# Kernel tuning notes

Measured on AMD Instinct MI355X. Metric: run time of the kernel, lower is better.

## Reference

```python
import jax, jax.numpy as jnp
import numpy as np

EPS = 1e-8
INV_SQRT = 1.0 / np.sqrt(1.0 + EPS)  # 1/sqrt(|k|+eps), |k|=1 for both hyp and sph


def layernorm(x, w, b, eps=1e-5):
    m = jnp.mean(x, axis=-1, keepdims=True)
    v = jnp.mean((x - m) ** 2, axis=-1, keepdims=True)
    return (x - m) * jax.lax.rsqrt(v + eps) * w + b


def setup_inputs() -> dict:
    key = jax.random.key(0)
    B, S, D, H = 4, 1024, 512, 8
    d = D // H
    FF = 2048
    ks = jax.random.split(key, 12)
    s_attn = 1.0 / np.sqrt(d)
    s_d = 1.0 / np.sqrt(D)
    s_ff = 1.0 / np.sqrt(FF)
    return {
        "x": jax.random.normal(ks[0], (B, S, D), jnp.float32),
        "Wq": jax.random.normal(ks[1], (H, d, d), jnp.float32) * s_attn,
        "Wk": jax.random.normal(ks[2], (H, d, d), jnp.float32) * s_attn,
        "Wv": jax.random.normal(ks[3], (H, d, d), jnp.float32) * s_attn,
        "gw": jnp.ones((H, 3), jnp.float32) / 3.0,
        "temp": jnp.ones((H,), jnp.float32),
        "Wo": jax.random.normal(ks[4], (D, D), jnp.float32) * s_d,
        "bo": jnp.zeros((D,), jnp.float32),
        "ln1_w": jnp.ones((D,), jnp.float32),
        "ln1_b": jnp.zeros((D,), jnp.float32),
        "ln2_w": jnp.ones((D,), jnp.float32),
        "ln2_b": jnp.zeros((D,), jnp.float32),
        "W1": jax.random.normal(ks[5], (FF, D), jnp.float32) * s_d,
        "b1": jnp.zeros((FF,), jnp.float32),
        "W2": jax.random.normal(ks[6], (D, FF), jnp.float32) * s_ff,
        "b2": jnp.zeros((D,), jnp.float32),
    }


def reference(x, Wq, Wk, Wv, gw, temp, Wo, bo, ln1_w, ln1_b, ln2_w, ln2_b, W1, b1, W2, b2):
    B, S, D = x.shape
    H = Wq.shape[0]
    d = D // H

    h = layernorm(x, ln1_w, ln1_b)
    xh = h.reshape(B, S, H, d).transpose(0, 2, 1, 3)  # [B,H,S,d]
    # nn.Linear: y = x @ W^T
    q = jnp.einsum("bhsd,hed->bhse", xh, Wq)
    k = jnp.einsum("bhsd,hed->bhse", xh, Wk)
    v = jnp.einsum("bhsd,hed->bhse", xh, Wv)

    qsq = jnp.sum(q * q, axis=-1)  # [B,H,S] == ||q||^2
    ksq = jnp.sum(k * k, axis=-1)
    qk = jnp.einsum("bhsd,bhtd->bhst", q, k)
    # ||q-k||^2 via expansion (same math as sum(diff^2), avoids [B,H,S,S,d])
    dsq = jnp.maximum(qsq[..., :, None] + ksq[..., None, :] - 2.0 * qk, 0.0)
    euc = jnp.sqrt(dsq + EPS)

    denom = (1.0 - qsq)[..., :, None] * (1.0 - ksq)[..., None, :] + EPS
    cosh_arg = jnp.clip(1.0 + 2.0 * dsq / denom, 1.0, 1e6)
    hyp = jnp.arccosh(cosh_arg) * INV_SQRT

    qn = jnp.sqrt(qsq)
    kn = jnp.sqrt(ksq)
    cos_angle = qk / ((qn + EPS)[..., :, None] * (kn + EPS)[..., None, :])
    cos_angle = jnp.clip(cos_angle, -1.0 + EPS, 1.0 - EPS)
    sph = jnp.arccos(cos_angle) * INV_SQRT

    w = jax.nn.softmax(gw, axis=-1)  # [H,3] per-head geometry mixing
    comb = (
        w[:, 0, None, None] * hyp
        + w[:, 1, None, None] * euc
        + w[:, 2, None, None] * sph
    )
    sim = -comb * temp[None, :, None, None]
    attn = jax.nn.softmax(sim, axis=-1)
    out = jnp.einsum("bhst,bhtd->bhsd", attn, v)
    out = out.transpose(0, 2, 1, 3).reshape(B, S, D)
    attn_out = out @ Wo.T + bo

    x = x + attn_out  # dropout=0 (eval)
    h2 = layernorm(x, ln2_w, ln2_b)
    ff = jax.nn.gelu(h2 @ W1.T + b1, approximate=False) @ W2.T + b2
    return x + ff, w
```

## Files before the change

kernel.cpp:

```cpp
#include <hip/hip_runtime.h>
#include <hip/hip_bf16.h>
#include <math.h>

typedef __attribute__((ext_vector_type(4))) float f32x4;
typedef __attribute__((ext_vector_type(8))) short bf16x8;
typedef unsigned short u16;
typedef unsigned int u32;

typedef f32x4  __attribute__((may_alias)) f32x4a;
typedef bf16x8 __attribute__((may_alias)) bf16x8a;
typedef uint2  __attribute__((may_alias)) uint2a;

__device__ __forceinline__ u16 bfbits(float f) {
  union { __hip_bfloat16 h; u16 u; } cv;
  cv.h = __float2bfloat16(f);
  return cv.u;
}
__device__ __forceinline__ float rcp_r(float x)  { return __builtin_amdgcn_rcpf(x); }
__device__ __forceinline__ float sqrt_r(float x) { return __builtin_amdgcn_sqrtf(x); }
__device__ __forceinline__ float log2_r(float x) { return __builtin_amdgcn_logf(x); }
__device__ __forceinline__ float exp2_r(float x) { return __builtin_amdgcn_exp2f(x); }
__device__ __forceinline__ float rsq_r(float x)  { return __builtin_amdgcn_rsqf(x); }
__device__ __forceinline__ u32 cvt_pk_bf16(float lo, float hi) {
  u32 r;
  asm("v_cvt_pk_bf16_f32 %0, %1, %2" : "=v"(r) : "v"(lo), "v"(hi));
  return r;
}
typedef const __attribute__((address_space(1))) unsigned int* gas_t;
typedef __attribute__((address_space(3))) unsigned int* las_t;
__device__ __forceinline__ void gload_lds16(const u16* g, u16* l) {
  __builtin_amdgcn_global_load_lds((gas_t)g, (las_t)l, 16, 0, 0);
}

__global__ __launch_bounds__(256) void convert_weights(
    const float* __restrict__ wq, const float* __restrict__ wk, const float* __restrict__ wv,
    const float* __restrict__ wo, const float* __restrict__ w1, const float* __restrict__ w2,
    u16* __restrict__ owq, u16* __restrict__ owk, u16* __restrict__ owv,
    u16* __restrict__ owo, u16* __restrict__ ow1, u16* __restrict__ ow2) {
  int i = blockIdx.x * 256 + threadIdx.x;
  const float* src; u16* dst; int base;
  if (i < 8192)        { src = wq; dst = owq; base = 0; }
  else if (i < 16384)  { src = wk; dst = owk; base = 8192; }
  else if (i < 24576)  { src = wv; dst = owv; base = 16384; }
  else if (i < 90112)  { src = wo; dst = owo; base = 24576; }
  else if (i < 352256) { src = w1; dst = ow1; base = 90112; }
  else                 { src = w2; dst = ow2; base = 352256; }
  int li = i - base;
  float4 v = reinterpret_cast<const float4*>(src)[li];
  ushort4 o;
  o.x = bfbits(v.x); o.y = bfbits(v.y); o.z = bfbits(v.z); o.w = bfbits(v.w);
  reinterpret_cast<ushort4*>(dst)[li] = o;
}

__global__ __launch_bounds__(128) void ln_kernel(const float* __restrict__ x,
    const float* __restrict__ w, const float* __restrict__ b, u16* __restrict__ out) {
  int row = blockIdx.x, tid = threadIdx.x;
  float4 v = reinterpret_cast<const float4*>(x + row * 512)[tid];
  float s  = v.x + v.y + v.z + v.w;
  float s2 = v.x*v.x + v.y*v.y + v.z*v.z + v.w*v.w;
  #pragma unroll
  for (int o = 32; o > 0; o >>= 1) { s += __shfl_down(s, o); s2 += __shfl_down(s2, o); }
  __shared__ float sm[4];
  if ((tid & 63) == 0) { sm[(tid >> 6)*2] = s; sm[(tid >> 6)*2 + 1] = s2; }
  __syncthreads();
  float ts = sm[0] + sm[2], ts2 = sm[1] + sm[3];
  float mean = ts * (1.f/512.f);
  float var  = ts2 * (1.f/512.f) - mean*mean;
  float rstd = rsq_r(var + 1e-5f);
  float4 wv = reinterpret_cast<const float4*>(w)[tid];
  float4 bv = reinterpret_cast<const float4*>(b)[tid];
  ushort4 o;
  o.x = bfbits((v.x-mean)*rstd*wv.x + bv.x);
  o.y = bfbits((v.y-mean)*rstd*wv.y + bv.y);
  o.z = bfbits((v.z-mean)*rstd*wv.z + bv.z);
  o.w = bfbits((v.w-mean)*rstd*wv.w + bv.w);
  reinterpret_cast<ushort4*>(out + row * 512)[tid] = o;
}

__global__ __launch_bounds__(256) void qkv_kernel(const u16* __restrict__ h1,
    const u16* __restrict__ wqb, const u16* __restrict__ wkb, const u16* __restrict__ wvb,
    u16* __restrict__ q, u16* __restrict__ k, u16* __restrict__ vt,
    float* __restrict__ qsq, float* __restrict__ qom, float* __restrict__ qrs,
    float* __restrict__ ksq, float* __restrict__ kom, float* __restrict__ krs) {
  int mt = blockIdx.x, head = blockIdx.y;
  int wave = threadIdx.x >> 6, lane = threadIdx.x & 63;
  int lr = lane & 15, lg = lane >> 4;
  int m0 = mt * 64 + wave * 16;
  __shared__ u16 qlds[4][16*72];
  const u16* xr = h1 + (m0 + lr) * 512 + head * 64 + lg * 8;
  bf16x8 a0 = *reinterpret_cast<const bf16x8a*>(xr);
  bf16x8 a1 = *reinterpret_cast<const bf16x8a*>(xr + 32);
  int bq = m0 >> 10;
  int s0 = m0 & 1023;
  int bh = (bq << 3) + head;
  #pragma unroll 1
  for (int mat = 0; mat < 3; ++mat) {
    const u16* W = (mat == 0 ? wqb : mat == 1 ? wkb : wvb) + head * 4096;
    f32x4 acc[4];
    #pragma unroll
    for (int c = 0; c < 4; c++)
      #pragma unroll
      for (int j = 0; j < 4; j++) acc[c][j] = 0.f;
    #pragma unroll
    for (int c = 0; c < 4; c++) {
      const u16* wr = W + (c*16 + lr) * 64 + lg * 8;
      bf16x8 b0 = *reinterpret_cast<const bf16x8a*>(wr);
      bf16x8 b1 = *reinterpret_cast<const bf16x8a*>(wr + 32);
      acc[c] = __builtin_amdgcn_mfma_f32_16x16x32_bf16(a0, b0, acc[c], 0, 0, 0);
      acc[c] = __builtin_amdgcn_mfma_f32_16x16x32_bf16(a1, b1, acc[c], 0, 0, 0);
    }
    if (mat == 2) {
      #pragma unroll
      for (int c = 0; c < 4; c++) {
        ushort4 st;
        st.x = bfbits(acc[c][0]); st.y = bfbits(acc[c][1]);
        st.z = bfbits(acc[c][2]); st.w = bfbits(acc[c][3]);
        *reinterpret_cast<ushort4*>(&vt[(bh*64 + c*16 + lr) * 1024 + s0 + 4*lg]) = st;
      }
    } else {
      u16* dst = (mat == 0 ? q : k);
      float* sq = (mat == 0 ? qsq : ksq);
      float* om = (mat == 0 ? qom : kom);
      float* rs = (mat == 0 ? qrs : krs);
      float ss[4] = {0.f, 0.f, 0.f, 0.f};
      u16* tile = &qlds[wave][0];
      #pragma unroll
      for (int c = 0; c < 4; c++)
        #pragma unroll
        for (int j = 0; j < 4; j++) {
          float vv = acc[c][j];
          tile[(4*lg + j)*72 + c*16 + lr] = bfbits(vv);
          ss[j] += vv * vv;
        }
      #pragma unroll
      for (int j = 0; j < 4; j++) {
        #pragma unroll
        for (int o = 1; o < 16; o <<= 1) ss[j] += __shfl_xor(ss[j], o);
      }
      if (lr == 0) {
        #pragma unroll
        for (int j = 0; j < 4; j++) {
          float v = ss[j];
          int idx = bh*1024 + s0 + 4*lg + j;
          sq[idx] = v;
          om[idx] = rcp_r(1.f - v);
          rs[idx] = rsq_r(v);
        }
      }
      int row = lane >> 2, ch = lane & 3;
      bf16x8 r0 = *reinterpret_cast<const bf16x8a*>(&tile[row*72 + ch*16]);
      bf16x8 r1 = *reinterpret_cast<const bf16x8a*>(&tile[row*72 + ch*16 + 8]);
      u16* dp = dst + (size_t)(bh*1024 + s0 + row)*64 + ch*16;
      *reinterpret_cast<bf16x8a*>(dp) = r0;
      *reinterpret_cast<bf16x8a*>(dp + 8) = r1;
    }
  }
}

__global__ __launch_bounds__(512, 4) void attn_kernel(
    const u16* __restrict__ q, const u16* __restrict__ k, const u16* __restrict__ vt,
    const float* __restrict__ qsqA, const float* __restrict__ qomA, const float* __restrict__ qrsA,
    const float* __restrict__ ksqA, const float* __restrict__ komA, const float* __restrict__ krsA,
    const float* __restrict__ gw, const float* __restrict__ temp,
    u16* __restrict__ attnb) {
  int bh = blockIdx.y;
  int b = bh >> 3, head = bh & 7;
  int tid = threadIdx.x;
  int wave = tid >> 6;
  int wq = wave & 1;
  int split = wave >> 1;
  int lane = tid & 63;
  int lr = lane & 15, lg = lane >> 4;
  int q0 = blockIdx.x * 32 + wq * 16;

  const u16* qp = q  + bh * 65536;
  const u16* kp = k  + bh * 65536;
  const u16* vp = vt + bh * 65536;

  __shared__ float ks_s[1024], kom_s[1024], rkn_s[1024];
  __shared__ __align__(16) u16 umem[5120];
  u16* pw = umem + wave * 640;

  for (int i = tid; i < 1024; i += 512) {
    ks_s[i]  = ksqA[(bh << 10) + i];
    kom_s[i] = komA[(bh << 10) + i];
    rkn_s[i] = krsA[(bh << 10) + i];
  }
  __syncthreads();

  float g0 = gw[head*3], g1 = gw[head*3+1], g2 = gw[head*3+2];
  float gm = fmaxf(g0, fmaxf(g1, g2));
  float e0 = __expf(g0-gm), e1 = __expf(g1-gm), e2 = __expf(g2-gm);
  float gi = rcp_r(e0 + e1 + e2);
  float tp = temp[head];
  const float LOG2E = 1.4426950408889634f;
  float chn = -e0*gi*tp;
  float cen = -e1*gi*tp*LOG2E;
  float csn = -e2*gi*tp*LOG2E;

  const u16* qr = qp + (q0 + lr) * 64 + lg * 8;
  bf16x8 aq0 = *reinterpret_cast<const bf16x8a*>(qr);
  bf16x8 aq1 = *reinterpret_cast<const bf16x8a*>(qr + 32);
  float qs   = qsqA[(bh << 10) + q0 + lr];
  float qom2 = 2.f * qomA[(bh << 10) + q0 + lr];
  float rqn  = qrsA[(bh << 10) + q0 + lr];

  f32x4 acc[4];
  #pragma unroll
  for (int c = 0; c < 4; c++)
    #pragma unroll
    for (int j = 0; j < 4; j++) acc[c][j] = 0.f;
  float psum0 = 0.f, psum1 = 0.f;

  for (int it = 0; it < 8; ++it) {
    int t0 = split * 256 + it * 32;
    const u16* kr = kp + (t0 + lr) * 64 + lg * 8;
    bf16x8 k00 = *reinterpret_cast<const bf16x8a*>(kr);
    bf16x8 k01 = *reinterpret_cast<const bf16x8a*>(kr + 32);
    bf16x8 k10 = *reinterpret_cast<const bf16x8a*>(kr + 1024);
    bf16x8 k11 = *reinterpret_cast<const bf16x8a*>(kr + 1024 + 32);
    f32x4 s0, s1;
    #pragma unroll
    for (int j = 0; j < 4; j++) { s0[j] = 0.f; s1[j] = 0.f; }
    s0 = __builtin_amdgcn_mfma_f32_16x16x32_bf16(k00, aq0, s0, 0, 0, 0);
    s0 = __builtin_amdgcn_mfma_f32_16x16x32_bf16(k01, aq1, s0, 0, 0, 0);
    s1 = __builtin_amdgcn_mfma_f32_16x16x32_bf16(k10, aq0, s1, 0, 0, 0);
    s1 = __builtin_amdgcn_mfma_f32_16x16x32_bf16(k11, aq1, s1, 0, 0, 0);

    f32x4 kq0 = *reinterpret_cast<const f32x4a*>(&ks_s[t0 + 4*lg]);
    f32x4 kq1 = *reinterpret_cast<const f32x4a*>(&ks_s[t0 + 16 + 4*lg]);
    f32x4 ko0 = *reinterpret_cast<const f32x4a*>(&kom_s[t0 + 4*lg]);
    f32x4 ko1 = *reinterpret_cast<const f32x4a*>(&kom_s[t0 + 16 + 4*lg]);
    f32x4 rk0 = *reinterpret_cast<const f32x4a*>(&rkn_s[t0 + 4*lg]);
    f32x4 rk1 = *reinterpret_cast<const f32x4a*>(&rkn_s[t0 + 16 + 4*lg]);

    float pv0[4], pv1[4];
    #pragma unroll
    for (int tc = 0; tc < 2; tc++) {
      f32x4 sv = tc ? s1 : s0;
      f32x4 kq = tc ? kq1 : kq0;
      f32x4 ko = tc ? ko1 : ko0;
      f32x4 rk = tc ? rk1 : rk0;
      float* pv = tc ? pv1 : pv0;
      #pragma unroll
      for (int j = 0; j < 4; j++) {
        float qk  = sv[j];
        float dsq = fmaxf(fmaf(qk, -2.f, qs + kq[j]), 0.f);
        float euc = sqrt_r(dsq);
        float u   = dsq * qom2 * ko[j];
        u = fminf(fmaxf(u, 0.f), 999999.f);
        float u2 = u + u;
        float sr = sqrt_r(fmaf(u, u, u2));
        float hyp2 = log2_r((u + 1.f) + sr);
        float ca = qk * rqn * rk[j];
        ca = fminf(fmaxf(ca, -1.f), 1.f);
        float aa = fabsf(ca);
        float pp = fmaf(aa, -0.0187293f, 0.0742610f);
        pp = fmaf(aa, pp, -0.2121144f);
        pp = fmaf(aa, pp, 1.5707288f);
        float rr = sqrt_r(1.f - aa) * pp;
        float sph = ca < 0.f ? 3.14159265358979f - rr : rr;
        float sim2 = fmaf(chn, hyp2, fmaf(cen, euc, csn * sph));
        float p = exp2_r(sim2);
        if (tc) psum1 += p; else psum0 += p;
        pv[j] = p;
      }
    }
    u32 w0 = cvt_pk_bf16(pv0[0], pv0[1]);
    u32 w1 = cvt_pk_bf16(pv0[2], pv0[3]);
    u32 w2 = cvt_pk_bf16(pv1[0], pv1[1]);
    u32 w3 = cvt_pk_bf16(pv1[2], pv1[3]);
    *reinterpret_cast<uint2a*>(pw + lr*40 + 4*lg)      = make_uint2(w0, w1);
    *reinterpret_cast<uint2a*>(pw + lr*40 + 16 + 4*lg) = make_uint2(w2, w3);
    bf16x8 pa = *reinterpret_cast<const bf16x8a*>(pw + lr*40 + lg*8);
    #pragma unroll
    for (int c = 0; c < 4; c++) {
      bf16x8 av = *reinterpret_cast<const bf16x8a*>(vp + (c*16 + lr)*1024 + t0 + lg*8);
      acc[c] = __builtin_amdgcn_mfma_f32_16x16x32_bf16(av, pa, acc[c], 0, 0, 0);
    }
  }

  float lt = psum0 + psum1;
  lt += __shfl_xor(lt, 16);
  lt += __shfl_xor(lt, 32);

  float* fa = (float*)umem;
  __syncthreads();
  #pragma unroll 1
  for (int s = 1; s <= 3; ++s) {
    int base = (wq*64 + lane)*20;
    if (split == s) {
      #pragma unroll
      for (int c = 0; c < 4; c++)
        *reinterpret_cast<f32x4a*>(fa + base + c*4) = acc[c];
      fa[base + 16] = lt;
    }
    __syncthreads();
    if (split == 0) {
      #pragma unroll
      for (int c = 0; c < 4; c++)
        acc[c] += *reinterpret_cast<const f32x4a*>(fa + base + c*4);
      lt += fa[base + 16];
    }
    __syncthreads();
  }
  if (split == 0) {
    float rl = rcp_r(lt);
    #pragma unroll
    for (int c = 0; c < 4; c++) {
      ushort4 st;
      st.x = bfbits(acc[c][0]*rl); st.y = bfbits(acc[c][1]*rl);
      st.z = bfbits(acc[c][2]*rl); st.w = bfbits(acc[c][3]*rl);
      *reinterpret_cast<ushort4*>(
          &attnb[(size_t)((b << 10) + q0 + lr) * 512 + head*64 + c*16 + 4*lg]) = st;
    }
  }
}

template<int K, int KS, int BM, int BN, int MODE>
__global__ __launch_bounds__(256, 2) void gemm_kernel(
    const u16* __restrict__ X, const u16* __restrict__ W,
    const float* __restrict__ bias, const float* __restrict__ res,
    float* __restrict__ outf, float* __restrict__ outf2, u16* __restrict__ outb) {
  constexpr int NS  = (MODE == 1) ? 2048 : 512;
  constexpr int WM  = (BM == 128 && BN == 128) ? 64 : 32;
  constexpr int WN  = (BN == 128 || BM == 128) ? 64 : 32;
  constexpr int NFR = WM / 16;
  constexpr int NFC = WN / 16;
  constexpr int NWC = BN / WN;
  constexpr int ACH = (BM * 4) / 256;
  constexpr int BCH = (BN * 4) / 256;
  __shared__ u16 As[BM * 32];
  __shared__ u16 Bs[BN * 32];
  int tid = threadIdx.x;
  int wave = tid >> 6, lane = tid & 63;
  int lr = lane & 15, lg = lane >> 4;
  int wr = (NWC == 2) ? (wave >> 1) : wave;
  int wc = (NWC == 2) ? (wave & 1) : 0;
  int m0 = blockIdx.x * BM, n0 = blockIdx.y * BN;
  const u16* Xp = X;
  const u16* Wp = W;
  if constexpr (MODE == 3) { Xp += blockIdx.z * K; Wp += blockIdx.z * K; }
  f32x4 acc[NFR][NFC];
  #pragma unroll
  for (int fr = 0; fr < NFR; fr++)
    #pragma unroll
    for (int fc = 0; fc < NFC; fc++)
      #pragma unroll
      for (int j = 0; j < 4; j++) acc[fr][fc][j] = 0.f;
  const u16* Ag[ACH]; u16* Al[ACH];
  const u16* Bg[BCH]; u16* Bl[BCH];
  #pragma unroll
  for (int i = 0; i < ACH; i++) {
    int cb = i * 256 + wave * 64;
    int c  = cb + lane;
    int row = c >> 2;
    int col = ((c & 3) ^ (row & 3)) << 3;
    Ag[i] = Xp + (size_t)(m0 + row) * KS + col;
    Al[i] = As + cb * 8;
  }
  #pragma unroll
  for (int i = 0; i < BCH; i++) {
    int cb = i * 256 + wave * 64;
    int c  = cb + lane;
    int row = c >> 2;
    int col = ((c & 3) ^ (row & 3)) << 3;
    Bg[i] = Wp + (size_t)(n0 + row) * KS + col;
    Bl[i] = Bs + cb * 8;
  }
  int rdcol = ((lg ^ (lr & 3)) << 3);
  for (int k0 = 0; k0 < K; k0 += 32) {
    __syncthreads();
    #pragma unroll
    for (int i = 0; i < ACH; i++) gload_lds16(Ag[i] + k0, Al[i]);
    #pragma unroll
    for (int i = 0; i < BCH; i++) gload_lds16(Bg[i] + k0, Bl[i]);
    __syncthreads();
    bf16x8 af[NFR], bf_[NFC];
    #pragma unroll
    for (int fr = 0; fr < NFR; fr++)
      af[fr] = *reinterpret_cast<const bf16x8a*>(As + (wr*WM + fr*16 + lr)*32 + rdcol);
    #pragma unroll
    for (int fc = 0; fc < NFC; fc++)
      bf_[fc] = *reinterpret_cast<const bf16x8a*>(Bs + (wc*WN + fc*16 + lr)*32 + rdcol);
    #pragma unroll
    for (int fr = 0; fr < NFR; fr++)
      #pragma unroll
      for (int fc = 0; fc < NFC; fc++)
        acc[fr][fc] = __builtin_amdgcn_mfma_f32_16x16x32_bf16(af[fr], bf_[fc], acc[fr][fc], 0, 0, 0);
  }
  float* po = nullptr;
  bool z0 = true;
  if constexpr (MODE == 3) { z0 = (blockIdx.z == 0); po = z0 ? outf : outf2; }
  #pragma unroll
  for (int fr = 0; fr < NFR; fr++)
    #pragma unroll
    for (int fc = 0; fc < NFC; fc++) {
      int col = n0 + wc*WN + fc*16 + lr;
      float bb = (MODE == 3) ? 0.f : bias[col];
      #pragma unroll
      for (int j = 0; j < 4; j++) {
        int row = m0 + wr*WM + fr*16 + 4*lg + j;
        float v = acc[fr][fc][j] + bb;
        if constexpr (MODE == 0) {
          outf[(size_t)row*NS + col] = v + res[(size_t)row*NS + col];
        } else if constexpr (MODE == 1) {
          float t = v * fmaf(v*v, 0.035677408137f, 0.7978845608f);
          float g = v * rcp_r(1.f + exp2_r(-2.8853900817779268f * t));
          outb[(size_t)row*NS + col] = bfbits(g);
        } else {
          if (z0) v += bias[col] + res[(size_t)row*512 + col];
          po[(size_t)row*512 + col] = v;
        }
      }
    }
}

__global__ __launch_bounds__(256) void ff2_combine(
    const float* __restrict__ p0, const float* __restrict__ p1,
    float* __restrict__ out, const float* __restrict__ gw, float* __restrict__ wout) {
  int i = blockIdx.x * 256 + threadIdx.x;
  float4 a = reinterpret_cast<const float4*>(p0)[i];
  float4 b = reinterpret_cast<const float4*>(p1)[i];
  float4 o;
  o.x = a.x + b.x;
  o.y = a.y + b.y;
  o.z = a.z + b.z;
  o.w = a.w + b.w;
  reinterpret_cast<float4*>(out)[i] = o;
  if (blockIdx.x == 0 && threadIdx.x < 8) {
    int h = threadIdx.x;
    float a0 = gw[h*3], a1 = gw[h*3+1], a2 = gw[h*3+2];
    float m = fmaxf(a0, fmaxf(a1, a2));
    float x0 = __expf(a0-m), x1 = __expf(a1-m), x2 = __expf(a2-m);
    float inv = rcp_r(x0 + x1 + x2);
    wout[h*3+0] = x0*inv; wout[h*3+1] = x1*inv; wout[h*3+2] = x2*inv;
  }
}

extern "C" void kernel_launch(void* const* d_in, const int* in_sizes, int n_in,
                              void* d_out, int out_size, void* d_ws, size_t ws_size,
                              hipStream_t stream) {
  const float* x    = (const float*)d_in[0];
  const float* Wq   = (const float*)d_in[1];
  const float* Wk   = (const float*)d_in[2];
  const float* Wv   = (const float*)d_in[3];
  const float* gw   = (const float*)d_in[4];
  const float* temp = (const float*)d_in[5];
  const float* Wo   = (const float*)d_in[6];
  const float* bo   = (const float*)d_in[7];
  const float* ln1w = (const float*)d_in[8];
  const float* ln1b = (const float*)d_in[9];
  const float* ln2w = (const float*)d_in[10];
  const float* ln2b = (const float*)d_in[11];
  const float* W1   = (const float*)d_in[12];
  const float* b1   = (const float*)d_in[13];
  const float* W2   = (const float*)d_in[14];
  const float* b2   = (const float*)d_in[15];

  char* ws = (char*)d_ws;
  u16*  wqb  = (u16*)(ws + 0);
  u16*  wkb  = (u16*)(ws + 65536);
  u16*  wvb  = (u16*)(ws + 131072);
  u16*  wob  = (u16*)(ws + 196608);
  u16*  w1b  = (u16*)(ws + 720896);
  u16*  w2b  = (u16*)(ws + 2818048);
  u16*  h1b  = (u16*)(ws + 4915200);
  u16*  qb   = (u16*)(ws + 9109504);
  u16*  kb   = (u16*)(ws + 13303808);
  u16*  vtb  = (u16*)(ws + 17498112);
  float* qsq = (float*)(ws + 21692416);
  float* ksq = (float*)(ws + 21823488);
  float* qom = (float*)(ws + 21954560);
  float* qrs = (float*)(ws + 22085632);
  float* kom = (float*)(ws + 22216704);
  float* krs = (float*)(ws + 22347776);
  u16*  attnb= (u16*)(ws + 22478848);
  float* x1  = (float*)(ws + 26673152);
  u16*  h2b  = (u16*)(ws + 35061760);
  float* p1f = (float*)(ws + 35061760);
  u16*  gb   = (u16*)(ws + 4915200);

  float* outf = (float*)d_out;
  float* wout = outf + 4096*512;

  convert_weights<<<2400, 256, 0, stream>>>(Wq, Wk, Wv, Wo, W1, W2,
                                            wqb, wkb, wvb, wob, w1b, w2b);
  ln_kernel<<<4096, 128, 0, stream>>>(x, ln1w, ln1b, h1b);
  qkv_kernel<<<dim3(64, 8), 256, 0, stream>>>(h1b, wqb, wkb, wvb, qb, kb, vtb,
                                              qsq, qom, qrs, ksq, kom, krs);
  attn_kernel<<<dim3(32, 32), 512, 0, stream>>>(qb, kb, vtb, qsq, qom, qrs,
                                                ksq, kom, krs, gw, temp, attnb);
  gemm_kernel<512, 512, 64, 64, 0><<<dim3(64, 8), 256, 0, stream>>>(
      attnb, wob, bo, x, x1, nullptr, nullptr);
  ln_kernel<<<4096, 128, 0, stream>>>(x1, ln2w, ln2b, h2b);
  gemm_kernel<512, 512, 128, 128, 1><<<dim3(32, 16), 256, 0, stream>>>(
      h2b, w1b, b1, nullptr, nullptr, nullptr, gb);
  gemm_kernel<1024, 2048, 128, 64, 3><<<dim3(32, 8, 2), 256, 0, stream>>>(
      gb, w2b, b2, x1, outf, p1f, nullptr);
  ff2_combine<<<2048, 256, 0, stream>>>(outf, p1f, outf, gw, wout);
}
```

Before: 229.8 us.

## Fuse Wo projection with LayerNorm2, merge prep kernels, drop FF2 split-K

Merges weight conversion, LayerNorm1 and the gate-weight softmax into one prep launch. Fuses the Wo GEMM with residual add and LayerNorm2 in a new kernel where each block computes 32 full rows of 512 columns. Replaces the split-K FF2 GEMM plus its combine kernel with a single full-K 64x64 GEMM. This cuts launches and a round trip of x1 and the partial sums through memory, but the fused Wo kernel runs only 128 blocks and FF2 loses its K-split parallelism.

```diff
diff --git a/kernel.cpp b/kernel.cpp
--- a/kernel.cpp
+++ b/kernel.cpp
@@ -32,49 +32,57 @@
   __builtin_amdgcn_global_load_lds((gas_t)g, (las_t)l, 16, 0, 0);
 }
 
-__global__ __launch_bounds__(256) void convert_weights(
+__global__ __launch_bounds__(256) void prep_kernel(
     const float* __restrict__ wq, const float* __restrict__ wk, const float* __restrict__ wv,
     const float* __restrict__ wo, const float* __restrict__ w1, const float* __restrict__ w2,
     u16* __restrict__ owq, u16* __restrict__ owk, u16* __restrict__ owv,
-    u16* __restrict__ owo, u16* __restrict__ ow1, u16* __restrict__ ow2) {
-  int i = blockIdx.x * 256 + threadIdx.x;
-  const float* src; u16* dst; int base;
-  if (i < 8192)        { src = wq; dst = owq; base = 0; }
-  else if (i < 16384)  { src = wk; dst = owk; base = 8192; }
-  else if (i < 24576)  { src = wv; dst = owv; base = 16384; }
-  else if (i < 90112)  { src = wo; dst = owo; base = 24576; }
-  else if (i < 352256) { src = w1; dst = ow1; base = 90112; }
-  else                 { src = w2; dst = ow2; base = 352256; }
-  int li = i - base;
-  float4 v = reinterpret_cast<const float4*>(src)[li];
-  ushort4 o;
-  o.x = bfbits(v.x); o.y = bfbits(v.y); o.z = bfbits(v.z); o.w = bfbits(v.w);
-  reinterpret_cast<ushort4*>(dst)[li] = o;
-}
-
-__global__ __launch_bounds__(128) void ln_kernel(const float* __restrict__ x,
-    const float* __restrict__ w, const float* __restrict__ b, u16* __restrict__ out) {
-  int row = blockIdx.x, tid = threadIdx.x;
-  float4 v = reinterpret_cast<const float4*>(x + row * 512)[tid];
-  float s  = v.x + v.y + v.z + v.w;
-  float s2 = v.x*v.x + v.y*v.y + v.z*v.z + v.w*v.w;
+    u16* __restrict__ owo, u16* __restrict__ ow1, u16* __restrict__ ow2,
+    const float* __restrict__ x, const float* __restrict__ ln1w, const float* __restrict__ ln1b,
+    u16* __restrict__ h1b, const float* __restrict__ gw, float* __restrict__ wout) {
+  int bid = blockIdx.x, tid = threadIdx.x;
+  if (bid < 2400) {
+    int i = bid * 256 + tid;
+    const float* src; u16* dst; int base;
+    if (i < 8192)        { src = wq; dst = owq; base = 0; }
+    else if (i < 16384)  { src = wk; dst = owk; base = 8192; }
+    else if (i < 24576)  { src = wv; dst = owv; base = 16384; }
+    else if (i < 90112)  { src = wo; dst = owo; base = 24576; }
+    else if (i < 352256) { src = w1; dst = ow1; base = 90112; }
+    else                 { src = w2; dst = ow2; base = 352256; }
+    int li = i - base;
+    float4 v = reinterpret_cast<const float4*>(src)[li];
+    ushort4 o;
+    o.x = bfbits(v.x); o.y = bfbits(v.y); o.z = bfbits(v.z); o.w = bfbits(v.w);
+    reinterpret_cast<ushort4*>(dst)[li] = o;
+    return;
+  }
+  int row = bid - 2400;
+  float2 v = reinterpret_cast<const float2*>(x + (size_t)row * 512)[tid];
+  float s  = v.x + v.y;
+  float s2 = v.x*v.x + v.y*v.y;
   #pragma unroll
   for (int o = 32; o > 0; o >>= 1) { s += __shfl_down(s, o); s2 += __shfl_down(s2, o); }
-  __shared__ float sm[4];
+  __shared__ float sm[8];
   if ((tid & 63) == 0) { sm[(tid >> 6)*2] = s; sm[(tid >> 6)*2 + 1] = s2; }
   __syncthreads();
-  float ts = sm[0] + sm[2], ts2 = sm[1] + sm[3];
+  float ts = sm[0]+sm[2]+sm[4]+sm[6], ts2 = sm[1]+sm[3]+sm[5]+sm[7];
   float mean = ts * (1.f/512.f);
   float var  = ts2 * (1.f/512.f) - mean*mean;
   float rstd = rsq_r(var + 1e-5f);
-  float4 wv = reinterpret_cast<const float4*>(w)[tid];
-  float4 bv = reinterpret_cast<const float4*>(b)[tid];
-  ushort4 o;
-  o.x = bfbits((v.x-mean)*rstd*wv.x + bv.x);
-  o.y = bfbits((v.y-mean)*rstd*wv.y + bv.y);
-  o.z = bfbits((v.z-mean)*rstd*wv.z + bv.z);
-  o.w = bfbits((v.w-mean)*rstd*wv.w + bv.w);
-  reinterpret_cast<ushort4*>(out + row * 512)[tid] = o;
+  float2 wv2 = reinterpret_cast<const float2*>(ln1w)[tid];
+  float2 bv2 = reinterpret_cast<const float2*>(ln1b)[tid];
+  ushort2 o2;
+  o2.x = bfbits((v.x-mean)*rstd*wv2.x + bv2.x);
+  o2.y = bfbits((v.y-mean)*rstd*wv2.y + bv2.y);
+  reinterpret_cast<ushort2*>(h1b + (size_t)row * 512)[tid] = o2;
+  if (row == 0 && tid < 8) {
+    int h = tid;
+    float a0 = gw[h*3], a1 = gw[h*3+1], a2 = gw[h*3+2];
+    float m = fmaxf(a0, fmaxf(a1, a2));
+    float x0 = __expf(a0-m), x1 = __expf(a1-m), x2 = __expf(a2-m);
+    float inv = rcp_r(x0 + x1 + x2);
+    wout[h*3+0] = x0*inv; wout[h*3+1] = x1*inv; wout[h*3+2] = x2*inv;
+  }
 }
 
 __global__ __launch_bounds__(256) void qkv_kernel(const u16* __restrict__ h1,
@@ -317,11 +325,102 @@
   }
 }
 
+__global__ __launch_bounds__(512) void wo_ln_kernel(
+    const u16* __restrict__ X, const u16* __restrict__ W,
+    const float* __restrict__ bo, const float* __restrict__ xres,
+    const float* __restrict__ ln2w, const float* __restrict__ ln2b,
+    float* __restrict__ x1, u16* __restrict__ h2b) {
+  __shared__ u16 As[32 * 32];
+  __shared__ u16 Bs[512 * 32];
+  __shared__ float lnr[32][4][2];
+  int tid = threadIdx.x;
+  int wave = tid >> 6, lane = tid & 63;
+  int lr = lane & 15, lg = lane >> 4;
+  int wr = wave >> 2, wc = wave & 3;
+  int m0 = blockIdx.x * 32;
+  f32x4 acc[8];
+  #pragma unroll
+  for (int fc = 0; fc < 8; fc++)
+    #pragma unroll
+    for (int j = 0; j < 4; j++) acc[fc][j] = 0.f;
+  int arow = tid >> 2;
+  int acol = ((tid & 3) ^ (arow & 3)) << 3;
+  const u16* Ag = X + (size_t)(m0 + (arow & 31)) * 512 + acol;
+  const u16* Bg[4];
+  #pragma unroll
+  for (int i = 0; i < 4; i++) {
+    int c = i*512 + tid;
+    int brow = c >> 2;
+    int bcol = ((c & 3) ^ (brow & 3)) << 3;
+    Bg[i] = W + (size_t)brow * 512 + bcol;
+  }
+  int rdcol = ((lg ^ (lr & 3)) << 3);
+  for (int k0 = 0; k0 < 512; k0 += 32) {
+    __syncthreads();
+    if (wave < 2) gload_lds16(Ag + k0, As + wave * 512);
+    #pragma unroll
+    for (int i = 0; i < 4; i++) gload_lds16(Bg[i] + k0, Bs + i*4096 + wave*512);
+    __syncthreads();
+    bf16x8 af = *reinterpret_cast<const bf16x8a*>(As + (wr*16 + lr)*32 + rdcol);
+    #pragma unroll
+    for (int fc = 0; fc < 8; fc++) {
+      bf16x8 bf_ = *reinterpret_cast<const bf16x8a*>(Bs + (wc*128 + fc*16 + lr)*32 + rdcol);
+      acc[fc] = __builtin_amdgcn_mfma_f32_16x16x32_bf16(af, bf_, acc[fc], 0, 0, 0);
+    }
+  }
+  float ps[4] = {0.f,0.f,0.f,0.f}, ps2[4] = {0.f,0.f,0.f,0.f};
+  #pragma unroll
+  for (int fc = 0; fc < 8; fc++) {
+    int col = wc*128 + fc*16 + lr;
+    float bb = bo[col];
+    #pragma unroll
+    for (int j = 0; j < 4; j++) {
+      int row = m0 + wr*16 + 4*lg + j;
+      float v = acc[fc][j] + bb + xres[(size_t)row*512 + col];
+      acc[fc][j] = v;
+      x1[(size_t)row*512 + col] = v;
+      ps[j] += v;
+      ps2[j] = fmaf(v, v, ps2[j]);
+    }
+  }
+  #pragma unroll
+  for (int j = 0; j < 4; j++) {
+    #pragma unroll
+    for (int o = 1; o < 16; o <<= 1) {
+      ps[j]  += __shfl_xor(ps[j], o);
+      ps2[j] += __shfl_xor(ps2[j], o);
+    }
+  }
+  if (lr == 0) {
+    #pragma unroll
+    for (int j = 0; j < 4; j++) {
+      int r = wr*16 + 4*lg + j;
+      lnr[r][wc][0] = ps[j];
+      lnr[r][wc][1] = ps2[j];
+    }
+  }
+  __syncthreads();
+  #pragma unroll
+  for (int j = 0; j < 4; j++) {
+    int r = wr*16 + 4*lg + j;
+    float ts  = lnr[r][0][0] + lnr[r][1][0] + lnr[r][2][0] + lnr[r][3][0];
+    float ts2 = lnr[r][0][1] + lnr[r][1][1] + lnr[r][2][1] + lnr[r][3][1];
+    float mean = ts * (1.f/512.f);
+    float rstd = rsq_r(ts2 * (1.f/512.f) - mean*mean + 1e-5f);
+    int row = m0 + r;
+    #pragma unroll
+    for (int fc = 0; fc < 8; fc++) {
+      int col = wc*128 + fc*16 + lr;
+      h2b[(size_t)row*512 + col] = bfbits((acc[fc][j] - mean)*rstd*ln2w[col] + ln2b[col]);
+    }
+  }
+}
+
 template<int K, int KS, int BM, int BN, int MODE>
 __global__ __launch_bounds__(256, 2) void gemm_kernel(
     const u16* __restrict__ X, const u16* __restrict__ W,
     const float* __restrict__ bias, const float* __restrict__ res,
-    float* __restrict__ outf, float* __restrict__ outf2, u16* __restrict__ outb) {
+    float* __restrict__ outf, u16* __restrict__ outb) {
   constexpr int NS  = (MODE == 1) ? 2048 : 512;
   constexpr int WM  = (BM == 128 && BN == 128) ? 64 : 32;
   constexpr int WN  = (BN == 128 || BM == 128) ? 64 : 32;
@@ -338,9 +437,6 @@
   int wr = (NWC == 2) ? (wave >> 1) : wave;
   int wc = (NWC == 2) ? (wave & 1) : 0;
   int m0 = blockIdx.x * BM, n0 = blockIdx.y * BN;
-  const u16* Xp = X;
-  const u16* Wp = W;
-  if constexpr (MODE == 3) { Xp += blockIdx.z * K; Wp += blockIdx.z * K; }
   f32x4 acc[NFR][NFC];
   #pragma unroll
   for (int fr = 0; fr < NFR; fr++)
@@ -356,7 +452,7 @@
     int c  = cb + lane;
     int row = c >> 2;
     int col = ((c & 3) ^ (row & 3)) << 3;
-    Ag[i] = Xp + (size_t)(m0 + row) * KS + col;
+    Ag[i] = X + (size_t)(m0 + row) * KS + col;
     Al[i] = As + cb * 8;
   }
   #pragma unroll
@@ -365,7 +461,7 @@
     int c  = cb + lane;
     int row = c >> 2;
     int col = ((c & 3) ^ (row & 3)) << 3;
-    Bg[i] = Wp + (size_t)(n0 + row) * KS + col;
+    Bg[i] = W + (size_t)(n0 + row) * KS + col;
     Bl[i] = Bs + cb * 8;
   }
   int rdcol = ((lg ^ (lr & 3)) << 3);
@@ -389,53 +485,25 @@
       for (int fc = 0; fc < NFC; fc++)
         acc[fr][fc] = __builtin_amdgcn_mfma_f32_16x16x32_bf16(af[fr], bf_[fc], acc[fr][fc], 0, 0, 0);
   }
-  float* po = nullptr;
-  bool z0 = true;
-  if constexpr (MODE == 3) { z0 = (blockIdx.z == 0); po = z0 ? outf : outf2; }
   #pragma unroll
   for (int fr = 0; fr < NFR; fr++)
     #pragma unroll
     for (int fc = 0; fc < NFC; fc++) {
       int col = n0 + wc*WN + fc*16 + lr;
-      float bb = (MODE == 3) ? 0.f : bias[col];
+      float bb = bias[col];
       #pragma unroll
       for (int j = 0; j < 4; j++) {
         int row = m0 + wr*WM + fr*16 + 4*lg + j;
         float v = acc[fr][fc][j] + bb;
         if constexpr (MODE == 0) {
           outf[(size_t)row*NS + col] = v + res[(size_t)row*NS + col];
-        } else if constexpr (MODE == 1) {
+        } else {
           float t = v * fmaf(v*v, 0.035677408137f, 0.7978845608f);
           float g = v * rcp_r(1.f + exp2_r(-2.8853900817779268f * t));
           outb[(size_t)row*NS + col] = bfbits(g);
-        } else {
-          if (z0) v += bias[col] + res[(size_t)row*512 + col];
-          po[(size_t)row*512 + col] = v;
         }
       }
     }
-}
-
-__global__ __launch_bounds__(256) void ff2_combine(
-    const float* __restrict__ p0, const float* __restrict__ p1,
-    float* __restrict__ out, const float* __restrict__ gw, float* __restrict__ wout) {
-  int i = blockIdx.x * 256 + threadIdx.x;
-  float4 a = reinterpret_cast<const float4*>(p0)[i];
-  float4 b = reinterpret_cast<const float4*>(p1)[i];
-  float4 o;
-  o.x = a.x + b.x;
-  o.y = a.y + b.y;
-  o.z = a.z + b.z;
-  o.w = a.w + b.w;
-  reinterpret_cast<float4*>(out)[i] = o;
-  if (blockIdx.x == 0 && threadIdx.x < 8) {
-    int h = threadIdx.x;
-    float a0 = gw[h*3], a1 = gw[h*3+1], a2 = gw[h*3+2];
-    float m = fmaxf(a0, fmaxf(a1, a2));
-    float x0 = __expf(a0-m), x1 = __expf(a1-m), x2 = __expf(a2-m);
-    float inv = rcp_r(x0 + x1 + x2);
-    wout[h*3+0] = x0*inv; wout[h*3+1] = x1*inv; wout[h*3+2] = x2*inv;
-  }
 }
 
 extern "C" void kernel_launch(void* const* d_in, const int* in_sizes, int n_in,
@@ -478,25 +546,21 @@
   u16*  attnb= (u16*)(ws + 22478848);
   float* x1  = (float*)(ws + 26673152);
   u16*  h2b  = (u16*)(ws + 35061760);
-  float* p1f = (float*)(ws + 35061760);
   u16*  gb   = (u16*)(ws + 4915200);
 
   float* outf = (float*)d_out;
   float* wout = outf + 4096*512;
 
-  convert_weights<<<2400, 256, 0, stream>>>(Wq, Wk, Wv, Wo, W1, W2,
-                                            wqb, wkb, wvb, wob, w1b, w2b);
-  ln_kernel<<<4096, 128, 0, stream>>>(x, ln1w, ln1b, h1b);
+  prep_kernel<<<2400 + 4096, 256, 0, stream>>>(
+      Wq, Wk, Wv, Wo, W1, W2, wqb, wkb, wvb, wob, w1b, w2b,
+      x, ln1w, ln1b, h1b, gw, wout);
   qkv_kernel<<<dim3(64, 8), 256, 0, stream>>>(h1b, wqb, wkb, wvb, qb, kb, vtb,
                                               qsq, qom, qrs, ksq, kom, krs);
   attn_kernel<<<dim3(32, 32), 512, 0, stream>>>(qb, kb, vtb, qsq, qom, qrs,
                                                 ksq, kom, krs, gw, temp, attnb);
-  gemm_kernel<512, 512, 64, 64, 0><<<dim3(64, 8), 256, 0, stream>>>(
-      attnb, wob, bo, x, x1, nullptr, nullptr);
-  ln_kernel<<<4096, 128, 0, stream>>>(x1, ln2w, ln2b, h2b);
+  wo_ln_kernel<<<128, 512, 0, stream>>>(attnb, wob, bo, x, ln2w, ln2b, x1, h2b);
   gemm_kernel<512, 512, 128, 128, 1><<<dim3(32, 16), 256, 0, stream>>>(
-      h2b, w1b, b1, nullptr, nullptr, nullptr, gb);
-  gemm_kernel<1024, 2048, 128, 64, 3><<<dim3(32, 8, 2), 256, 0, stream>>>(
-      gb, w2b, b2, x1, outf, p1f, nullptr);
-  ff2_combine<<<2048, 256, 0, stream>>>(outf, p1f, outf, gw, wout);
-}
+      h2b, w1b, b1, nullptr, nullptr, gb);
+  gemm_kernel<2048, 2048, 64, 64, 0><<<dim3(64, 8), 256, 0, stream>>>(
+      gb, w2b, b2, x1, outf, nullptr);
+}
```

New measurement: 234.0 us. Within noise of the previous version (+1.8%).
